# Kernel tuning notes

Measured on AMD Instinct MI355X. Metric: run time of the kernel, lower is better.

## Reference

```python
import jax, jax.numpy as jnp
import numpy as np

D_MODEL = 1024
NUM_HEADS = 16
D_K = D_MODEL // NUM_HEADS


def setup_inputs() -> dict:
    key = jax.random.key(0)
    ks = jax.random.split(key, 9)
    s = 1.0 / np.sqrt(D_MODEL)
    inp = {
        'x': jax.random.normal(ks[0], (1, 4096, D_MODEL), dtype=jnp.float32),
        'W_q': jax.random.uniform(ks[1], (D_MODEL, D_MODEL), jnp.float32, -s, s),
        'b_q': jax.random.uniform(ks[2], (D_MODEL,), jnp.float32, -s, s),
        'W_k': jax.random.uniform(ks[3], (D_MODEL, D_MODEL), jnp.float32, -s, s),
        'b_k': jax.random.uniform(ks[4], (D_MODEL,), jnp.float32, -s, s),
        'W_v': jax.random.uniform(ks[5], (D_MODEL, D_MODEL), jnp.float32, -s, s),
        'b_v': jax.random.uniform(ks[6], (D_MODEL,), jnp.float32, -s, s),
        'W_o': jax.random.uniform(ks[7], (D_MODEL, D_MODEL), jnp.float32, -s, s),
        'b_o': jax.random.uniform(ks[8], (D_MODEL,), jnp.float32, -s, s),
    }
    return inp


def reference(x, W_q, b_q, W_k, b_k, W_v, b_v, W_o, b_o):
    B, S, _ = x.shape
    def split_heads(t):  # [B,S,D] -> [B,H,S,d_k]
        return t.reshape(B, S, NUM_HEADS, D_K).transpose(0, 2, 1, 3)
    Q = split_heads(x @ W_q + b_q)
    K = split_heads(x @ W_k + b_k)
    V = split_heads(x @ W_v + b_v)
    scale = 1.0 / jnp.sqrt(jnp.float32(D_K))
    scores = jnp.einsum('bhqd,bhkd->bhqk', Q, K) * scale  # [B,H,S,S]
    attn = jax.nn.softmax(scores, axis=-1)
    ctx = jnp.einsum('bhqk,bhkd->bhqd', attn, V)
    ctx = ctx.transpose(0, 2, 1, 3).reshape(B, S, D_MODEL)
    return ctx @ W_o + b_o
```

## Files before the change

kernel.cpp:

```cpp
#include <hip/hip_runtime.h>
#include <hip/hip_bf16.h>
#include <stdint.h>


#define DM 1024
#define SEQ 4096
#define NH 16
#define DK 64

#define QSCALE 0.18033688011112042f

typedef __attribute__((ext_vector_type(8))) short bf16x8;
typedef __attribute__((ext_vector_type(4))) float f32x4;
typedef __attribute__((ext_vector_type(2))) uint32_t u32x2;

__device__ __forceinline__ short f2bf(float f) {
  union { float f; uint32_t u; } x; x.f = f;
  uint32_t r = x.u + 0x7fffu + ((x.u >> 16) & 1u);
  return (short)(r >> 16);
}

__device__ __forceinline__ void gl_lds16(const void* g, void* l) {
  __builtin_amdgcn_global_load_lds(
      (const __attribute__((address_space(1))) void*)g,
      (__attribute__((address_space(3))) void*)l, 16, 0, 0);
}

__global__ __launch_bounds__(256) void cvt_x_k(const float* __restrict__ in,
                                               short* __restrict__ out) {
  size_t i = (size_t)blockIdx.x * 256 + threadIdx.x;
  const float4* ip = (const float4*)in;
  float4 a = ip[2 * i], b = ip[2 * i + 1];
  bf16x8 o;
  o[0] = f2bf(a.x); o[1] = f2bf(a.y); o[2] = f2bf(a.z); o[3] = f2bf(a.w);
  o[4] = f2bf(b.x); o[5] = f2bf(b.y); o[6] = f2bf(b.z); o[7] = f2bf(b.w);
  *(bf16x8*)(out + 8 * i) = o;
}

__global__ __launch_bounds__(256) void cvt_wt_k(const float* __restrict__ W0,
                                                const float* __restrict__ W1,
                                                const float* __restrict__ W2,
                                                const float* __restrict__ W3,
                                                short* __restrict__ Wt0) {
  __shared__ alignas(16) short T[64][66];
  const int z = blockIdx.z;
  const float* W = (z == 0) ? W0 : (z == 1) ? W1 : (z == 2) ? W2 : W3;
  short* Wt = Wt0 + (size_t)z * (DM * DM);
  const int k0 = blockIdx.y * 64, n0 = blockIdx.x * 64;
#pragma unroll
  for (int rep = 0; rep < 16; ++rep) {
    int lin = rep * 256 + threadIdx.x;
    int i = lin >> 6, j = lin & 63;
    T[i][j] = f2bf(W[(size_t)(k0 + i) * DM + n0 + j]);
  }
  __syncthreads();
#pragma unroll
  for (int rep = 0; rep < 16; ++rep) {
    int lin = rep * 256 + threadIdx.x;
    int n = lin >> 6, kk = lin & 63;
    Wt[(size_t)(n0 + n) * DM + k0 + kk] = T[kk][n];
  }
}

__global__ __launch_bounds__(256) void trans_v_k(const short* __restrict__ V,
                                                 short* __restrict__ Vt) {
  __shared__ alignas(16) short T[64][66];
  const int s0 = blockIdx.x * 64, h = blockIdx.y;
#pragma unroll
  for (int rep = 0; rep < 16; ++rep) {
    int lin = rep * 256 + threadIdx.x;
    int i = lin >> 6, j = lin & 63;
    T[i][j] = V[(size_t)(s0 + i) * DM + h * DK + j];
  }
  __syncthreads();
#pragma unroll
  for (int rep = 0; rep < 16; ++rep) {
    int lin = rep * 256 + threadIdx.x;
    int d = lin >> 6, ss = lin & 63;
    int sp = ((ss & 15) << 2) + (ss >> 4);
    Vt[((size_t)h * DK + d) * SEQ + s0 + sp] = T[ss][d];
  }
}

__global__ __launch_bounds__(256) void gemm_qkv(
    const short* __restrict__ xb, const short* __restrict__ Wt0,
    const float* __restrict__ bq, const float* __restrict__ bk,
    const float* __restrict__ bv, short* __restrict__ out0) {
  const int z = blockIdx.z;
  const short* Bt = Wt0 + (size_t)z * (DM * DM);
  const float* bias = (z == 0) ? bq : (z == 1) ? bk : bv;
  const float qs = (z == 0) ? QSCALE : 1.0f;
  short* out = out0 + (size_t)z * ((size_t)SEQ * DM);

  __shared__ alignas(16) short As[128 * 32];
  __shared__ alignas(16) short Bs[128 * 32];
  const int tid = threadIdx.x, lane = tid & 63, w = tid >> 6;
  const int bm = blockIdx.y * 128, bn = blockIdx.x * 128;
  const int wm = (w >> 1) * 64, wn = (w & 1) * 64;
  f32x4 acc[4][4] = {};

  for (int kt = 0; kt < DM; kt += 32) {
    __syncthreads();
#pragma unroll
    for (int c = 0; c < 2; ++c) {
      int i = w * 2 + c;
      int ob = i * 1024 + lane * 16;
      int row = ob >> 6, colb = ob & 63;
      gl_lds16((const char*)xb + ((size_t)(bm + row) * DM + kt) * 2 + colb,
               (char*)As + i * 1024);
      gl_lds16((const char*)Bt + ((size_t)(bn + row) * DM + kt) * 2 + colb,
               (char*)Bs + i * 1024);
    }
    __syncthreads();
    bf16x8 bfr[4];
#pragma unroll
    for (int n = 0; n < 4; ++n)
      bfr[n] = *(const bf16x8*)((const char*)Bs +
                                (wn + n * 16 + (lane & 15)) * 64 + (lane >> 4) * 16);
#pragma unroll
    for (int m = 0; m < 4; ++m) {
      bf16x8 af = *(const bf16x8*)((const char*)As +
                                   (wm + m * 16 + (lane & 15)) * 64 + (lane >> 4) * 16);
#pragma unroll
      for (int n = 0; n < 4; ++n)
        acc[m][n] = __builtin_amdgcn_mfma_f32_16x16x32_bf16(af, bfr[n], acc[m][n], 0, 0, 0);
    }
  }
  const int r0 = bm + wm + ((lane >> 4) << 2);
  const int c0 = bn + wn + (lane & 15);
#pragma unroll
  for (int n = 0; n < 4; ++n) {
    const int col = c0 + n * 16;
    const float b = bias[col];
#pragma unroll
    for (int m = 0; m < 4; ++m)
#pragma unroll
      for (int r = 0; r < 4; ++r)
        out[(size_t)(r0 + m * 16 + r) * DM + col] = f2bf((acc[m][n][r] + b) * qs);
  }
}

__global__ __launch_bounds__(256) void gemm_out(
    const short* __restrict__ A, const short* __restrict__ Bt,
    const float* __restrict__ bias, float* __restrict__ out) {
  __shared__ alignas(16) short As[128 * 32];
  __shared__ alignas(16) short Bs[128 * 32];
  const int tid = threadIdx.x, lane = tid & 63, w = tid >> 6;
  const int bm = blockIdx.y * 128, bn = blockIdx.x * 128;
  const int wm = (w >> 1) * 64, wn = (w & 1) * 64;
  f32x4 acc[4][4] = {};

  for (int kt = 0; kt < DM; kt += 32) {
    __syncthreads();
#pragma unroll
    for (int c = 0; c < 2; ++c) {
      int i = w * 2 + c;
      int ob = i * 1024 + lane * 16;
      int row = ob >> 6, colb = ob & 63;
      gl_lds16((const char*)A + ((size_t)(bm + row) * DM + kt) * 2 + colb,
               (char*)As + i * 1024);
      gl_lds16((const char*)Bt + ((size_t)(bn + row) * DM + kt) * 2 + colb,
               (char*)Bs + i * 1024);
    }
    __syncthreads();
    bf16x8 bfr[4];
#pragma unroll
    for (int n = 0; n < 4; ++n)
      bfr[n] = *(const bf16x8*)((const char*)Bs +
                                (wn + n * 16 + (lane & 15)) * 64 + (lane >> 4) * 16);
#pragma unroll
    for (int m = 0; m < 4; ++m) {
      bf16x8 af = *(const bf16x8*)((const char*)As +
                                   (wm + m * 16 + (lane & 15)) * 64 + (lane >> 4) * 16);
#pragma unroll
      for (int n = 0; n < 4; ++n)
        acc[m][n] = __builtin_amdgcn_mfma_f32_16x16x32_bf16(af, bfr[n], acc[m][n], 0, 0, 0);
    }
  }
  const int r0 = bm + wm + ((lane >> 4) << 2);
  const int c0 = bn + wn + (lane & 15);
#pragma unroll
  for (int n = 0; n < 4; ++n) {
    const int col = c0 + n * 16;
    const float b = bias[col];
#pragma unroll
    for (int m = 0; m < 4; ++m)
#pragma unroll
      for (int r = 0; r < 4; ++r)
        out[(size_t)(r0 + m * 16 + r) * DM + col] = acc[m][n][r] + b;
  }
}

__global__ __launch_bounds__(256) void attn_k(
    const short* __restrict__ Qb, const short* __restrict__ Kb,
    const short* __restrict__ Vt, short* __restrict__ ctx) {
  const int h = blockIdx.y, qt = blockIdx.x;
  const int tid = threadIdx.x, lane = tid & 63, w = tid >> 6;
  __shared__ alignas(16) short Ks[2][64 * 64];
  __shared__ alignas(16) short Vs[2][64 * 64];
  __shared__ alignas(16) short Pl[4][16 * 64];

  const int qr = qt * 64 + w * 16 + (lane & 15);
  const short* qp = Qb + (size_t)qr * DM + h * DK + ((lane >> 4) * 8);
  const bf16x8 qf0 = *(const bf16x8*)qp;
  const bf16x8 qf1 = *(const bf16x8*)(qp + 32);

  bf16x8 ones;
#pragma unroll
  for (int j = 0; j < 8; ++j) ones[j] = (short)0x3F80;

  f32x4 o[4] = {};
  f32x4 ol = {};
  float m = -3000.f;

  const int xk = (lane & 7) << 4;
  char* pbase = (char*)&Pl[w][0];
  const int g = lane >> 4, cl = lane & 15;

  auto stage = [&](int buf, int s0) {
#pragma unroll
    for (int c = 0; c < 2; ++c) {
      int i = w * 2 + c;
      int ob = i * 1024 + lane * 16;
      int row = ob >> 7, colb = ob & 127;
      int src = colb ^ ((row & 7) << 4);
      gl_lds16((const char*)Kb + ((size_t)(s0 + row) * DM + h * DK) * 2 + src,
               (char*)&Ks[buf][0] + i * 1024);
      gl_lds16((const char*)Vt + ((size_t)(h * DK + row) * SEQ + s0) * 2 + src,
               (char*)&Vs[buf][0] + i * 1024);
    }
  };

  stage(0, 0);

  for (int t = 0; t < SEQ / 64; ++t) {
    const int cur = t & 1;
    __syncthreads();
    if (t < SEQ / 64 - 1) stage(cur ^ 1, (t + 1) * 64);

    const char* kbase = (const char*)&Ks[cur][0];
    const char* vbase = (const char*)&Vs[cur][0];

    f32x4 sc[4] = {};
    __builtin_amdgcn_s_setprio(1);
#pragma unroll
    for (int kk = 0; kk < 2; ++kk) {
      bf16x8 a = kk ? qf1 : qf0;
#pragma unroll
      for (int n = 0; n < 4; ++n) {
        bf16x8 b = *(const bf16x8*)(kbase + (n * 16 + cl) * 128 +
                                    ((kk * 64 + g * 16) ^ xk));
        sc[n] = __builtin_amdgcn_mfma_f32_16x16x32_bf16(a, b, sc[n], 0, 0, 0);
      }
    }
    __builtin_amdgcn_s_setprio(0);

    float lm = fmaxf(fmaxf(fmaxf(sc[0][0], sc[0][1]), fmaxf(sc[0][2], sc[0][3])),
                     fmaxf(fmaxf(sc[1][0], sc[1][1]), fmaxf(sc[1][2], sc[1][3])));
    lm = fmaxf(lm, fmaxf(fmaxf(fmaxf(sc[2][0], sc[2][1]), fmaxf(sc[2][2], sc[2][3])),
                         fmaxf(fmaxf(sc[3][0], sc[3][1]), fmaxf(sc[3][2], sc[3][3]))));
    lm = fmaxf(lm, __shfl_xor(lm, 1));
    lm = fmaxf(lm, __shfl_xor(lm, 2));
    lm = fmaxf(lm, __shfl_xor(lm, 4));
    lm = fmaxf(lm, __shfl_xor(lm, 8));
    if (!__all(lm <= m + 8.f)) {
      float mn = fmaxf(m, lm);
      float al = exp2f(m - mn);
      m = mn;
#pragma unroll
      for (int n = 0; n < 4; ++n) {
        o[n][0] *= al; o[n][1] *= al; o[n][2] *= al; o[n][3] *= al;
      }
      ol[0] *= al; ol[1] *= al; ol[2] *= al; ol[3] *= al;
    }

#pragma unroll
    for (int r = 0; r < 4; ++r) {
      const int prow = g * 4 + r;
      float p0 = exp2f(sc[0][r] - m), p1 = exp2f(sc[1][r] - m);
      float p2 = exp2f(sc[2][r] - m), p3 = exp2f(sc[3][r] - m);
      uint32_t u0, u1;
      asm("v_cvt_pk_bf16_f32 %0, %1, %2" : "=v"(u0) : "v"(p0), "v"(p1));
      asm("v_cvt_pk_bf16_f32 %0, %1, %2" : "=v"(u1) : "v"(p2), "v"(p3));
      u32x2 uu; uu[0] = u0; uu[1] = u1;
      *(u32x2*)(pbase + prow * 128 + ((cl * 8) ^ ((prow & 7) << 4))) = uu;
    }

    __builtin_amdgcn_s_setprio(1);
#pragma unroll
    for (int kk = 0; kk < 2; ++kk) {
      bf16x8 pa = *(const bf16x8*)(pbase + cl * 128 + ((kk * 64 + g * 16) ^ xk));
      ol = __builtin_amdgcn_mfma_f32_16x16x32_bf16(pa, ones, ol, 0, 0, 0);
#pragma unroll
      for (int n = 0; n < 4; ++n) {
        bf16x8 vb = *(const bf16x8*)(vbase + (n * 16 + cl) * 128 +
                                     ((kk * 64 + g * 16) ^ xk));
        o[n] = __builtin_amdgcn_mfma_f32_16x16x32_bf16(pa, vb, o[n], 0, 0, 0);
      }
    }
    __builtin_amdgcn_s_setprio(0);
  }

#pragma unroll
  for (int r = 0; r < 4; ++r) {
    float inv = 1.f / ol[r];
    int row = qt * 64 + w * 16 + g * 4 + r;
#pragma unroll
    for (int n = 0; n < 4; ++n)
      ctx[(size_t)row * DM + h * DK + n * 16 + cl] = f2bf(o[n][r] * inv);
  }
}

extern "C" void kernel_launch(void* const* d_in, const int* in_sizes, int n_in,
                              void* d_out, int out_size, void* d_ws, size_t ws_size,
                              hipStream_t stream) {
  const float* x  = (const float*)d_in[0];
  const float* Wq = (const float*)d_in[1];
  const float* bq = (const float*)d_in[2];
  const float* Wk = (const float*)d_in[3];
  const float* bk = (const float*)d_in[4];
  const float* Wv = (const float*)d_in[5];
  const float* bv = (const float*)d_in[6];
  const float* Wo = (const float*)d_in[7];
  const float* bo = (const float*)d_in[8];

  char* ws = (char*)d_ws;
  short* xb  = (short*)(ws + (size_t)0);
  short* Wt  = (short*)(ws + ((size_t)8 << 20));
  short* Qb  = (short*)(ws + ((size_t)16 << 20));
  short* Kb  = (short*)(ws + ((size_t)24 << 20));
  short* Vb  = (short*)(ws + ((size_t)32 << 20));
  short* Vt  = (short*)(ws + ((size_t)40 << 20));
  short* ctx = (short*)(ws + ((size_t)48 << 20));

  cvt_x_k<<<2048, 256, 0, stream>>>(x, xb);
  cvt_wt_k<<<dim3(16, 16, 4), 256, 0, stream>>>(Wq, Wk, Wv, Wo, Wt);
  gemm_qkv<<<dim3(DM / 128, SEQ / 128, 3), 256, 0, stream>>>(xb, Wt, bq, bk, bv, Qb);
  trans_v_k<<<dim3(SEQ / 64, NH), 256, 0, stream>>>(Vb, Vt);
  attn_k<<<dim3(SEQ / 64, NH), 256, 0, stream>>>(Qb, Kb, Vt, ctx);
  gemm_out<<<dim3(DM / 128, SEQ / 128), 256, 0, stream>>>(
      ctx, Wt + (size_t)3 * (DM * DM), bo, (float*)d_out);
}
```

Measured before the change: 291.4 us.

## Rewrite attention with 32x32x16 MFMA, register-resident P and 2-wave blocks

The attention kernel switches from 16x16x32 MFMAs to 32x32x16 MFMAs computing S^T = K·Q^T, so each lane owns one query row. P now stays in registers and is exchanged across half-waves with ds_bpermute instead of a round trip through LDS. The row-sum comes from register adds rather than an MFMA against a ones vector, and the running max is folded into the accumulator init. Blocks shrink to 2 waves of 32 rows each with launch bounds for two blocks per CU, and the V transpose drops its column permutation to match the new layout. The aim is fewer LDS accesses and instructions per tile, at the cost of higher register pressure and fewer waves per block.

Measured after the change: 294.0 us. No clear change (+0.9%).

```diff
diff --git a/kernel.cpp b/kernel.cpp
--- a/kernel.cpp
+++ b/kernel.cpp
@@ -12,7 +12,9 @@
 
 typedef __attribute__((ext_vector_type(8))) short bf16x8;
 typedef __attribute__((ext_vector_type(4))) float f32x4;
+typedef __attribute__((ext_vector_type(16))) float f32x16;
 typedef __attribute__((ext_vector_type(2))) uint32_t u32x2;
+typedef __attribute__((ext_vector_type(4))) uint32_t u32x4;
 
 __device__ __forceinline__ short f2bf(float f) {
   union { float f; uint32_t u; } x; x.f = f;
@@ -24,6 +26,16 @@
   __builtin_amdgcn_global_load_lds(
       (const __attribute__((address_space(1))) void*)g,
       (__attribute__((address_space(3))) void*)l, 16, 0, 0);
+}
+
+__device__ __forceinline__ uint32_t cvtpk(float lo, float hi) {
+  uint32_t r;
+  asm("v_cvt_pk_bf16_f32 %0, %1, %2" : "=v"(r) : "v"(lo), "v"(hi));
+  return r;
+}
+
+__device__ __forceinline__ uint32_t xlane(uint32_t v, int lane) {
+  return (uint32_t)__builtin_amdgcn_ds_bpermute(((lane ^ 32) << 2), (int)v);
 }
 
 __global__ __launch_bounds__(256) void cvt_x_k(const float* __restrict__ in,
@@ -77,8 +89,7 @@
   for (int rep = 0; rep < 16; ++rep) {
     int lin = rep * 256 + threadIdx.x;
     int d = lin >> 6, ss = lin & 63;
-    int sp = ((ss & 15) << 2) + (ss >> 4);
-    Vt[((size_t)h * DK + d) * SEQ + s0 + sp] = T[ss][d];
+    Vt[((size_t)h * DK + d) * SEQ + s0 + ss] = T[ss][d];
   }
 }
 
@@ -191,123 +202,144 @@
   }
 }
 
-__global__ __launch_bounds__(256) void attn_k(
+__global__ __launch_bounds__(128, 2) void attn_k(
     const short* __restrict__ Qb, const short* __restrict__ Kb,
     const short* __restrict__ Vt, short* __restrict__ ctx) {
   const int h = blockIdx.y, qt = blockIdx.x;
   const int tid = threadIdx.x, lane = tid & 63, w = tid >> 6;
   __shared__ alignas(16) short Ks[2][64 * 64];
   __shared__ alignas(16) short Vs[2][64 * 64];
-  __shared__ alignas(16) short Pl[4][16 * 64];
-
-  const int qr = qt * 64 + w * 16 + (lane & 15);
-  const short* qp = Qb + (size_t)qr * DM + h * DK + ((lane >> 4) * 8);
-  const bf16x8 qf0 = *(const bf16x8*)qp;
-  const bf16x8 qf1 = *(const bf16x8*)(qp + 32);
-
-  bf16x8 ones;
-#pragma unroll
-  for (int j = 0; j < 8; ++j) ones[j] = (short)0x3F80;
-
-  f32x4 o[4] = {};
-  f32x4 ol = {};
-  float m = -3000.f;
-
-  const int xk = (lane & 7) << 4;
-  char* pbase = (char*)&Pl[w][0];
-  const int g = lane >> 4, cl = lane & 15;
+
+  const int cq = lane & 31, hh = lane >> 5;
+  const int qrow = qt * 64 + w * 32 + cq;
+
+  bf16x8 qf[4];
+  {
+    const short* qp = Qb + (size_t)qrow * DM + h * DK + hh * 8;
+#pragma unroll
+    for (int ks = 0; ks < 4; ++ks) qf[ks] = *(const bf16x8*)(qp + ks * 16);
+  }
+
+  f32x16 o0 = {}, o1 = {};
+  float ol = 0.f;
+  f32x16 mv;
+#pragma unroll
+  for (int j = 0; j < 16; ++j) mv[j] = 3000.f;
+
+  const int rsw = (cq & 7) << 4;
 
   auto stage = [&](int buf, int s0) {
 #pragma unroll
-    for (int c = 0; c < 2; ++c) {
-      int i = w * 2 + c;
-      int ob = i * 1024 + lane * 16;
-      int row = ob >> 7, colb = ob & 127;
-      int src = colb ^ ((row & 7) << 4);
+    for (int c = 0; c < 4; ++c) {
+      int row = 16 * c + 8 * w + (lane >> 3);
+      int src = (((lane & 7) ^ (lane >> 3)) << 4);
       gl_lds16((const char*)Kb + ((size_t)(s0 + row) * DM + h * DK) * 2 + src,
-               (char*)&Ks[buf][0] + i * 1024);
+               (char*)&Ks[buf][0] + w * 1024 + c * 2048);
       gl_lds16((const char*)Vt + ((size_t)(h * DK + row) * SEQ + s0) * 2 + src,
-               (char*)&Vs[buf][0] + i * 1024);
+               (char*)&Vs[buf][0] + w * 1024 + c * 2048);
     }
   };
 
   stage(0, 0);
-
-  for (int t = 0; t < SEQ / 64; ++t) {
+  const int NT = SEQ / 64;
+  for (int t = 0; t < NT; ++t) {
     const int cur = t & 1;
     __syncthreads();
-    if (t < SEQ / 64 - 1) stage(cur ^ 1, (t + 1) * 64);
-
-    const char* kbase = (const char*)&Ks[cur][0];
-    const char* vbase = (const char*)&Vs[cur][0];
-
-    f32x4 sc[4] = {};
+    if (t < NT - 1) stage(cur ^ 1, (t + 1) * 64);
+    const char* kb = (const char*)&Ks[cur][0];
+    const char* vb = (const char*)&Vs[cur][0];
+
+    f32x16 s0v, s1v;
     __builtin_amdgcn_s_setprio(1);
-#pragma unroll
-    for (int kk = 0; kk < 2; ++kk) {
-      bf16x8 a = kk ? qf1 : qf0;
-#pragma unroll
-      for (int n = 0; n < 4; ++n) {
-        bf16x8 b = *(const bf16x8*)(kbase + (n * 16 + cl) * 128 +
-                                    ((kk * 64 + g * 16) ^ xk));
-        sc[n] = __builtin_amdgcn_mfma_f32_16x16x32_bf16(a, b, sc[n], 0, 0, 0);
+    {
+      bf16x8 kf = *(const bf16x8*)(kb + cq * 128 + ((hh * 16) ^ rsw));
+      s0v = __builtin_amdgcn_mfma_f32_32x32x16_bf16(kf, qf[0], mv, 0, 0, 0);
+      bf16x8 kg = *(const bf16x8*)(kb + (32 + cq) * 128 + ((hh * 16) ^ rsw));
+      s1v = __builtin_amdgcn_mfma_f32_32x32x16_bf16(kg, qf[0], mv, 0, 0, 0);
+    }
+#pragma unroll
+    for (int ks = 1; ks < 4; ++ks) {
+      bf16x8 kf = *(const bf16x8*)(kb + cq * 128 + ((ks * 32 + hh * 16) ^ rsw));
+      s0v = __builtin_amdgcn_mfma_f32_32x32x16_bf16(kf, qf[ks], s0v, 0, 0, 0);
+      bf16x8 kg = *(const bf16x8*)(kb + (32 + cq) * 128 + ((ks * 32 + hh * 16) ^ rsw));
+      s1v = __builtin_amdgcn_mfma_f32_32x32x16_bf16(kg, qf[ks], s1v, 0, 0, 0);
+    }
+    __builtin_amdgcn_s_setprio(0);
+
+    float mx[16];
+#pragma unroll
+    for (int j = 0; j < 16; ++j) mx[j] = fmaxf(s0v[j], s1v[j]);
+#pragma unroll
+    for (int sstep = 8; sstep > 0; sstep >>= 1)
+#pragma unroll
+      for (int j = 0; j < sstep; ++j) mx[j] = fmaxf(mx[j], mx[j + sstep]);
+    float lm = fmaxf(mx[0], __shfl_xor(mx[0], 32));
+
+    if (!__all(lm <= 8.f)) {
+      float dm = fmaxf(lm, 0.f);
+      float al = exp2f(-dm);
+#pragma unroll
+      for (int j = 0; j < 16; ++j) {
+        s0v[j] -= dm; s1v[j] -= dm;
+        o0[j] *= al;  o1[j] *= al;
+        mv[j] -= dm;
       }
+      ol *= al;
+    }
+
+    float p0[16], p1[16];
+#pragma unroll
+    for (int j = 0; j < 16; ++j) { p0[j] = exp2f(s0v[j]); p1[j] = exp2f(s1v[j]); }
+    float sm[16];
+#pragma unroll
+    for (int j = 0; j < 16; ++j) sm[j] = p0[j] + p1[j];
+#pragma unroll
+    for (int sstep = 8; sstep > 0; sstep >>= 1)
+#pragma unroll
+      for (int j = 0; j < sstep; ++j) sm[j] += sm[j + sstep];
+    ol += sm[0];
+
+    uint32_t pk[16];
+#pragma unroll
+    for (int c = 0; c < 4; ++c) {
+      pk[c * 2 + 0] = cvtpk(p0[4 * c + 0], p0[4 * c + 1]);
+      pk[c * 2 + 1] = cvtpk(p0[4 * c + 2], p0[4 * c + 3]);
+      pk[(4 + c) * 2 + 0] = cvtpk(p1[4 * c + 0], p1[4 * c + 1]);
+      pk[(4 + c) * 2 + 1] = cvtpk(p1[4 * c + 2], p1[4 * c + 3]);
+    }
+
+    __builtin_amdgcn_s_setprio(1);
+#pragma unroll
+    for (int ks = 0; ks < 4; ++ks) {
+      uint32_t a0 = pk[(2 * ks) * 2 + 0], a1 = pk[(2 * ks) * 2 + 1];
+      uint32_t b0 = pk[(2 * ks + 1) * 2 + 0], b1 = pk[(2 * ks + 1) * 2 + 1];
+      uint32_t ca0 = xlane(a0, lane), ca1 = xlane(a1, lane);
+      uint32_t cb0 = xlane(b0, lane), cb1 = xlane(b1, lane);
+      union { u32x4 u; bf16x8 b; } pf;
+      pf.u[0] = hh ? cb0 : a0;
+      pf.u[1] = hh ? cb1 : a1;
+      pf.u[2] = hh ? b0 : ca0;
+      pf.u[3] = hh ? b1 : ca1;
+      bf16x8 vf0 = *(const bf16x8*)(vb + cq * 128 + ((ks * 32 + hh * 16) ^ rsw));
+      o0 = __builtin_amdgcn_mfma_f32_32x32x16_bf16(vf0, pf.b, o0, 0, 0, 0);
+      bf16x8 vf1 = *(const bf16x8*)(vb + (32 + cq) * 128 + ((ks * 32 + hh * 16) ^ rsw));
+      o1 = __builtin_amdgcn_mfma_f32_32x32x16_bf16(vf1, pf.b, o1, 0, 0, 0);
     }
     __builtin_amdgcn_s_setprio(0);
-
-    float lm = fmaxf(fmaxf(fmaxf(sc[0][0], sc[0][1]), fmaxf(sc[0][2], sc[0][3])),
-                     fmaxf(fmaxf(sc[1][0], sc[1][1]), fmaxf(sc[1][2], sc[1][3])));
-    lm = fmaxf(lm, fmaxf(fmaxf(fmaxf(sc[2][0], sc[2][1]), fmaxf(sc[2][2], sc[2][3])),
-                         fmaxf(fmaxf(sc[3][0], sc[3][1]), fmaxf(sc[3][2], sc[3][3]))));
-    lm = fmaxf(lm, __shfl_xor(lm, 1));
-    lm = fmaxf(lm, __shfl_xor(lm, 2));
-    lm = fmaxf(lm, __shfl_xor(lm, 4));
-    lm = fmaxf(lm, __shfl_xor(lm, 8));
-    if (!__all(lm <= m + 8.f)) {
-      float mn = fmaxf(m, lm);
-      float al = exp2f(m - mn);
-      m = mn;
-#pragma unroll
-      for (int n = 0; n < 4; ++n) {
-        o[n][0] *= al; o[n][1] *= al; o[n][2] *= al; o[n][3] *= al;
-      }
-      ol[0] *= al; ol[1] *= al; ol[2] *= al; ol[3] *= al;
-    }
-
-#pragma unroll
-    for (int r = 0; r < 4; ++r) {
-      const int prow = g * 4 + r;
-      float p0 = exp2f(sc[0][r] - m), p1 = exp2f(sc[1][r] - m);
-      float p2 = exp2f(sc[2][r] - m), p3 = exp2f(sc[3][r] - m);
-      uint32_t u0, u1;
-      asm("v_cvt_pk_bf16_f32 %0, %1, %2" : "=v"(u0) : "v"(p0), "v"(p1));
-      asm("v_cvt_pk_bf16_f32 %0, %1, %2" : "=v"(u1) : "v"(p2), "v"(p3));
-      u32x2 uu; uu[0] = u0; uu[1] = u1;
-      *(u32x2*)(pbase + prow * 128 + ((cl * 8) ^ ((prow & 7) << 4))) = uu;
-    }
-
-    __builtin_amdgcn_s_setprio(1);
-#pragma unroll
-    for (int kk = 0; kk < 2; ++kk) {
-      bf16x8 pa = *(const bf16x8*)(pbase + cl * 128 + ((kk * 64 + g * 16) ^ xk));
-      ol = __builtin_amdgcn_mfma_f32_16x16x32_bf16(pa, ones, ol, 0, 0, 0);
-#pragma unroll
-      for (int n = 0; n < 4; ++n) {
-        bf16x8 vb = *(const bf16x8*)(vbase + (n * 16 + cl) * 128 +
-                                     ((kk * 64 + g * 16) ^ xk));
-        o[n] = __builtin_amdgcn_mfma_f32_16x16x32_bf16(pa, vb, o[n], 0, 0, 0);
-      }
-    }
-    __builtin_amdgcn_s_setprio(0);
-  }
-
-#pragma unroll
-  for (int r = 0; r < 4; ++r) {
-    float inv = 1.f / ol[r];
-    int row = qt * 64 + w * 16 + g * 4 + r;
-#pragma unroll
-    for (int n = 0; n < 4; ++n)
-      ctx[(size_t)row * DM + h * DK + n * 16 + cl] = f2bf(o[n][r] * inv);
+  }
+
+  float inv = 1.f / (ol + __shfl_xor(ol, 32));
+  short* cp = ctx + (size_t)qrow * DM + h * DK;
+#pragma unroll
+  for (int rg = 0; rg < 4; ++rg) {
+    int d0 = 8 * rg + 4 * hh;
+    u32x2 w0, w1;
+    w0[0] = cvtpk(o0[4 * rg + 0] * inv, o0[4 * rg + 1] * inv);
+    w0[1] = cvtpk(o0[4 * rg + 2] * inv, o0[4 * rg + 3] * inv);
+    *(u32x2*)(cp + d0) = w0;
+    w1[0] = cvtpk(o1[4 * rg + 0] * inv, o1[4 * rg + 1] * inv);
+    w1[1] = cvtpk(o1[4 * rg + 2] * inv, o1[4 * rg + 3] * inv);
+    *(u32x2*)(cp + 32 + d0) = w1;
   }
 }
 
@@ -337,7 +369,7 @@
   cvt_wt_k<<<dim3(16, 16, 4), 256, 0, stream>>>(Wq, Wk, Wv, Wo, Wt);
   gemm_qkv<<<dim3(DM / 128, SEQ / 128, 3), 256, 0, stream>>>(xb, Wt, bq, bk, bv, Qb);
   trans_v_k<<<dim3(SEQ / 64, NH), 256, 0, stream>>>(Vb, Vt);
-  attn_k<<<dim3(SEQ / 64, NH), 256, 0, stream>>>(Qb, Kb, Vt, ctx);
+  attn_k<<<dim3(SEQ / 64, NH), 128, 0, stream>>>(Qb, Kb, Vt, ctx);
   gemm_out<<<dim3(DM / 128, SEQ / 128), 256, 0, stream>>>(
       ctx, Wt + (size_t)3 * (DM * DM), bo, (float*)d_out);
 }
```
